# Kernel optimization log

Measured on AMD Instinct MI355X. Metric: run time of the kernel, lower is better.

The kernel has to match this reference:

```python
import jax, jax.numpy as jnp
import numpy as np

DEPTH = 6
DIM = 512
HEADS = 8
HD = DIM // HEADS          # head_dim = 64
HALF = HD // 4             # RoPE2D half_dim = 16
N = 85                     # 1 CLS + 4 + 16 + 64
TOKENS = [1, 4, 16, 64]
MAX_FREQ = 10.0
NEG = -1e30


def _build_mask():
    bounds = np.cumsum([0] + TOKENS)
    M = np.array([[1, 0, 0, 1], [1, 1, 0, 0], [1, 0, 1, 0], [0, 0, 0, 1]])
    m = np.full((N, N), NEG, np.float32)
    for i in range(4):
        for j in range(4):
            if M[i, j]:
                m[bounds[i]:bounds[i + 1], bounds[j]:bounds[j + 1]] = 0.0
    return jnp.asarray(m)

MASK = _build_mask()
FREQS = jnp.exp(jnp.arange(HALF, dtype=jnp.float32) * (-np.log(MAX_FREQ) / HALF))


def _centers():
    allc = []
    for g in (2, 4, 8):
        step = 1.0 / g
        off = step / 2
        ys, xs = np.meshgrid(np.arange(g), np.arange(g), indexing='ij')
        c = np.stack([off + xs * step, off + ys * step], axis=-1).reshape(-1, 2)
        allc.append(c)
    return jnp.asarray(np.concatenate(allc, 0), dtype=jnp.float32)


def _ln(x, w, b):
    mu = x.mean(-1, keepdims=True)
    var = x.var(-1, keepdims=True)
    return (x - mu) / jnp.sqrt(var + 1e-5) * w + b


def _rope(t, coords):
    # t: [B, H, M, HD] patch tokens (CLS excluded); coords: [M, 2]
    two_pi = 2.0 * jnp.pi
    ang_x = coords[:, 0:1] * FREQS[None, :] * two_pi   # [M, HALF]
    ang_y = coords[:, 1:2] * FREQS[None, :] * two_pi
    cx, sx = jnp.cos(ang_x), jnp.sin(ang_x)
    cy, sy = jnp.cos(ang_y), jnp.sin(ang_y)
    t = t.reshape(t.shape[:-1] + (4, HALF))
    x0, x1, x2, x3 = t[..., 0, :], t[..., 1, :], t[..., 2, :], t[..., 3, :]
    r = jnp.stack([x0 * cx - x1 * sx, x0 * sx + x1 * cx,
                   x2 * cy - x3 * sy, x2 * sy + x3 * cy], axis=-2)
    return r.reshape(r.shape[:-2] + (HD,))


def _attn(x, coords, qkv_w, qkv_b, proj_w, proj_b):
    B = x.shape[0]
    qkv = (x @ qkv_w + qkv_b).reshape(B, N, 3, HEADS, HD).transpose(2, 0, 3, 1, 4)
    q, k, v = qkv[0], qkv[1], qkv[2]   # each [B, H, N, HD]
    q = jnp.concatenate([q[:, :, :1], _rope(q[:, :, 1:], coords)], axis=2)
    k = jnp.concatenate([k[:, :, :1], _rope(k[:, :, 1:], coords)], axis=2)
    scores = jnp.einsum('bhqd,bhkd->bhqk', q, k) * (HD ** -0.5) + MASK
    a = jax.nn.softmax(scores, axis=-1)
    out = jnp.einsum('bhqk,bhkd->bhqd', a, v).transpose(0, 2, 1, 3).reshape(B, N, DIM)
    return out @ proj_w + proj_b


def _forward(x, coords, ln1_w, ln1_b, qkv_w, qkv_b, proj_w, proj_b,
             ln2_w, ln2_b, fc1_w, fc1_b, fc2_w, fc2_b, lnf_w, lnf_b):
    for l in range(DEPTH):
        h = _ln(x, ln1_w[l], ln1_b[l])
        x = x + _attn(h, coords, qkv_w[l], qkv_b[l], proj_w[l], proj_b[l])
        h = _ln(x, ln2_w[l], ln2_b[l])
        h = jax.nn.gelu(h @ fc1_w[l] + fc1_b[l], approximate=False)  # torch nn.GELU = erf
        x = x + h @ fc2_w[l] + fc2_b[l]
    return _ln(x, lnf_w, lnf_b)


def setup_inputs() -> dict:
    key = jax.random.key(0)
    ks = jax.random.split(key, 5)
    B = 512
    def w(k, shape, s=0.02):
        return jax.random.normal(k, shape, jnp.float32) * s
    return {
        'x': jax.random.normal(ks[0], (B, N, DIM), jnp.float32),
        'coords': _centers(),
        'ln1_w': jnp.ones((DEPTH, DIM), jnp.float32),
        'ln1_b': jnp.zeros((DEPTH, DIM), jnp.float32),
        'qkv_w': w(ks[1], (DEPTH, DIM, 3 * DIM)),
        'qkv_b': jnp.zeros((DEPTH, 3 * DIM), jnp.float32),
        'proj_w': w(ks[2], (DEPTH, DIM, DIM)),
        'proj_b': jnp.zeros((DEPTH, DIM), jnp.float32),
        'ln2_w': jnp.ones((DEPTH, DIM), jnp.float32),
        'ln2_b': jnp.zeros((DEPTH, DIM), jnp.float32),
        'fc1_w': w(ks[3], (DEPTH, DIM, 4 * DIM)),
        'fc1_b': jnp.zeros((DEPTH, 4 * DIM), jnp.float32),
        'fc2_w': w(ks[4], (DEPTH, 4 * DIM, DIM)),
        'fc2_b': jnp.zeros((DEPTH, DIM), jnp.float32),
        'lnf_w': jnp.ones((DIM,), jnp.float32),
        'lnf_b': jnp.zeros((DIM,), jnp.float32),
    }


def reference(x, coords, ln1_w, ln1_b, qkv_w, qkv_b, proj_w, proj_b,
              ln2_w, ln2_b, fc1_w, fc1_b, fc2_w, fc2_b, lnf_w, lnf_b):
    return _forward(x, coords, ln1_w, ln1_b, qkv_w, qkv_b, proj_w, proj_b,
                    ln2_w, ln2_b, fc1_w, fc1_b, fc2_w, fc2_b, lnf_w, lnf_b)
```

## Files before the change

### kernel.cpp

```cpp
#include <hip/hip_runtime.h>
#include <hip/hip_bf16.h>

typedef unsigned short u16;
typedef unsigned int u32;
typedef __attribute__((ext_vector_type(8))) short short8;
typedef __attribute__((ext_vector_type(4))) float floatx4;

#define MTOT 43520
#define DIMM 512
#define NHEAD 8

__device__ __forceinline__ float b2f(u16 u) { return __uint_as_float(((unsigned)u) << 16); }
__device__ __forceinline__ u16 f2b(float f) {
  unsigned u = __float_as_uint(f);
  return (u16)((u + 0x7FFFu + ((u >> 16) & 1u)) >> 16);
}

__device__ __forceinline__ void gld16(void* lds, const void* g) {
  __builtin_amdgcn_global_load_lds(
      (const __attribute__((address_space(1))) u32*)g,
      (__attribute__((address_space(3))) u32*)lds, 16, 0, 0);
}

__global__ __launch_bounds__(256) void transpose_conv(const float* __restrict__ in,
    u16* __restrict__ out, int K, int N)
{
  const float* W  = in  + (size_t)blockIdx.z * K * N;
  u16*         Wt = out + (size_t)blockIdx.z * K * N;
  int n0 = blockIdx.x * 64, k0 = blockIdx.y * 64;
  int t = threadIdx.x;
  #pragma unroll
  for (int i = 0; i < 2; i++) {
    int task = t + i * 256;
    int n = task >> 3, kc = (task & 7) * 8;
    u16 tmp[8];
    #pragma unroll
    for (int j = 0; j < 8; j++)
      tmp[j] = f2b(W[(size_t)(k0 + kc + j) * N + n0 + n]);
    *(uint4*)&Wt[(size_t)(n0 + n) * K + k0 + kc] = *(uint4*)tmp;
  }
}

template<int OUTF32>
__global__ __launch_bounds__(256) void ln_kernel(const float* __restrict__ x,
    const float* __restrict__ w, const float* __restrict__ b, void* __restrict__ out)
{
  int row  = blockIdx.x * 4 + (threadIdx.x >> 6);
  int lane = threadIdx.x & 63;
  const float* xr = x + (size_t)row * DIMM;
  float4 a = ((const float4*)xr)[lane * 2];
  float4 c = ((const float4*)xr)[lane * 2 + 1];
  float f[8] = { a.x, a.y, a.z, a.w, c.x, c.y, c.z, c.w };

  float s = 0.f, ss = 0.f;
  #pragma unroll
  for (int i = 0; i < 8; i++) { s += f[i]; ss += f[i] * f[i]; }
  #pragma unroll
  for (int off = 32; off > 0; off >>= 1) {
    s  += __shfl_xor(s,  off);
    ss += __shfl_xor(ss, off);
  }
  float mu  = s * (1.f / 512.f);
  float var = ss * (1.f / 512.f) - mu * mu;
  float rs  = rsqrtf(var + 1e-5f);

  float4 w0 = ((const float4*)w)[lane * 2], w1 = ((const float4*)w)[lane * 2 + 1];
  float4 b0 = ((const float4*)b)[lane * 2], b1 = ((const float4*)b)[lane * 2 + 1];
  float wv[8] = { w0.x, w0.y, w0.z, w0.w, w1.x, w1.y, w1.z, w1.w };
  float bv[8] = { b0.x, b0.y, b0.z, b0.w, b1.x, b1.y, b1.z, b1.w };

  if (OUTF32) {
    float res[8];
    #pragma unroll
    for (int i = 0; i < 8; i++) res[i] = (f[i] - mu) * rs * wv[i] + bv[i];
    float* orow = (float*)out + (size_t)row * DIMM;
    ((float4*)orow)[lane * 2]     = *(float4*)&res[0];
    ((float4*)orow)[lane * 2 + 1] = *(float4*)&res[4];
  } else {
    u16 res[8];
    #pragma unroll
    for (int i = 0; i < 8; i++) res[i] = f2b((f[i] - mu) * rs * wv[i] + bv[i]);
    ((uint4*)((u16*)out + (size_t)row * DIMM))[lane] = *(uint4*)res;
  }
}

template<int EPI>
__global__ __launch_bounds__(512, 2) void gemm256(
    const u16* __restrict__ A, const u16* __restrict__ Bt,
    const float* __restrict__ bias, const float* __restrict__ resid,
    void* __restrict__ Cv, int Nd, int K, int gx)
{
  __shared__ u16 As[2][2][128][64];
  __shared__ u16 Bs[2][2][128][64];

  int nwg  = gridDim.x;
  int orig = blockIdx.x;
  int xcd = orig & 7, cidx = orig >> 3;
  int qq = nwg >> 3, rr8 = nwg & 7;
  int nid = (xcd < rr8 ? xcd * (qq + 1) : rr8 * (qq + 1) + (xcd - rr8) * qq) + cidx;
  int bx = nid % gx, by = nid / gx;
  int m0 = by * 256, n0 = bx * 256;

  int t = threadIdx.x;
  int w = t >> 6, l = t & 63;
  int wr = w >> 2, wc = w & 3, quad = l >> 4, l16 = l & 15;
  int KT = K >> 6;

  int Rb = 8 * w + (l >> 3);
  int slog8 = (((l & 7) ^ ((l >> 3) & 7)) << 3);
  const u16* gAm = A  + (size_t)m0 * K + slog8;
  const u16* gBn = Bt + (size_t)n0 * K + slog8;
  int sx = l16 & 7;

  auto STAGE = [&](int ktj, int h) {
    int c = ktj & 1;
    u16* lb = (h < 2) ? &As[c][h & 1][0][0] : &Bs[c][h & 1][0][0];
    const u16* g = ((h < 2) ? gAm : gBn) + (size_t)((h & 1) * 128 + Rb) * K + ktj * 64;
    gld16(lb + w * 512,       g);
    gld16(lb + (8 + w) * 512, g + (size_t)64 * K);
  };

  STAGE(0, 0); STAGE(0, 1); STAGE(0, 2); STAGE(0, 3);
  STAGE(1, 0); STAGE(1, 1);
  asm volatile("s_waitcnt vmcnt(4)" ::: "memory");
  __builtin_amdgcn_s_barrier();
  __builtin_amdgcn_sched_barrier(0);

  floatx4 zero = {0.f, 0.f, 0.f, 0.f};
  floatx4 acc[8][4];
  #pragma unroll
  for (int mt = 0; mt < 8; mt++)
    #pragma unroll
    for (int nt = 0; nt < 4; nt++) acc[mt][nt] = zero;

  for (int kt = 0; kt < KT; ++kt) {
    int c = kt & 1;
    const u16 (*Ah)[64] = As[c][wr];
    const u16 (*Bh)[64] = Bs[c][wc >> 1];
    int bl = (wc & 1) * 64;

    short8 af[8][2], bf[4][2];

    #pragma unroll
    for (int mt = 0; mt < 4; mt++)
      #pragma unroll
      for (int kk = 0; kk < 2; kk++)
        af[mt][kk] = *(const short8*)&Ah[mt * 16 + l16][((kk * 4 + quad) ^ sx) << 3];
    #pragma unroll
    for (int nt = 0; nt < 2; nt++)
      #pragma unroll
      for (int kk = 0; kk < 2; kk++)
        bf[nt][kk] = *(const short8*)&Bh[bl + nt * 16 + l16][((kk * 4 + quad) ^ sx) << 3];
    { int j = 4 * kt + 6; if (j < 4 * KT) STAGE(j >> 2, j & 3); }
    __builtin_amdgcn_s_barrier();
    __builtin_amdgcn_s_setprio(1);
    #pragma unroll
    for (int nt = 0; nt < 2; nt++)
      #pragma unroll
      for (int mt = 0; mt < 4; mt++)
        #pragma unroll
        for (int kk = 0; kk < 2; kk++)
          acc[mt][nt] = __builtin_amdgcn_mfma_f32_16x16x32_bf16(af[mt][kk], bf[nt][kk], acc[mt][nt], 0, 0, 0);
    __builtin_amdgcn_s_setprio(0);
    __builtin_amdgcn_s_barrier();

    #pragma unroll
    for (int mt = 4; mt < 8; mt++)
      #pragma unroll
      for (int kk = 0; kk < 2; kk++)
        af[mt][kk] = *(const short8*)&Ah[mt * 16 + l16][((kk * 4 + quad) ^ sx) << 3];
    #pragma unroll
    for (int nt = 2; nt < 4; nt++)
      #pragma unroll
      for (int kk = 0; kk < 2; kk++)
        bf[nt][kk] = *(const short8*)&Bh[bl + nt * 16 + l16][((kk * 4 + quad) ^ sx) << 3];
    { int j = 4 * kt + 7; if (j < 4 * KT) STAGE(j >> 2, j & 3); }
    __builtin_amdgcn_s_barrier();
    __builtin_amdgcn_s_setprio(1);
    #pragma unroll
    for (int nt = 2; nt < 4; nt++)
      #pragma unroll
      for (int mt = 4; mt < 8; mt++)
        #pragma unroll
        for (int kk = 0; kk < 2; kk++)
          acc[mt][nt] = __builtin_amdgcn_mfma_f32_16x16x32_bf16(af[mt][kk], bf[nt][kk], acc[mt][nt], 0, 0, 0);
    __builtin_amdgcn_s_setprio(0);
    __builtin_amdgcn_s_barrier();

    { int j = 4 * kt + 8; if (j < 4 * KT) STAGE(j >> 2, j & 3); }
    __builtin_amdgcn_s_barrier();
    __builtin_amdgcn_s_setprio(1);
    #pragma unroll
    for (int nt = 2; nt < 4; nt++)
      #pragma unroll
      for (int mt = 0; mt < 4; mt++)
        #pragma unroll
        for (int kk = 0; kk < 2; kk++)
          acc[mt][nt] = __builtin_amdgcn_mfma_f32_16x16x32_bf16(af[mt][kk], bf[nt][kk], acc[mt][nt], 0, 0, 0);
    __builtin_amdgcn_s_setprio(0);
    __builtin_amdgcn_s_barrier();

    { int j = 4 * kt + 9; if (j < 4 * KT) STAGE(j >> 2, j & 3); }
    __builtin_amdgcn_s_barrier();
    __builtin_amdgcn_s_setprio(1);
    #pragma unroll
    for (int nt = 0; nt < 2; nt++)
      #pragma unroll
      for (int mt = 4; mt < 8; mt++)
        #pragma unroll
        for (int kk = 0; kk < 2; kk++)
          acc[mt][nt] = __builtin_amdgcn_mfma_f32_16x16x32_bf16(af[mt][kk], bf[nt][kk], acc[mt][nt], 0, 0, 0);
    __builtin_amdgcn_s_setprio(0);

    if (kt < KT - 1) {
      if (kt == KT - 2) asm volatile("s_waitcnt vmcnt(0)" ::: "memory");
      else              asm volatile("s_waitcnt vmcnt(4)" ::: "memory");
      __builtin_amdgcn_s_barrier();
      __builtin_amdgcn_sched_barrier(0);
    }
  }

  #pragma unroll
  for (int mt = 0; mt < 8; mt++) {
    #pragma unroll
    for (int nt = 0; nt < 4; nt++) {
      int nc = n0 + wc * 64 + nt * 16 + l16;
      float bv = bias[nc];
      #pragma unroll
      for (int r = 0; r < 4; r++) {
        int mr = m0 + wr * 128 + mt * 16 + quad * 4 + r;
        size_t idx = (size_t)mr * Nd + nc;
        float v = acc[mt][nt][r] + bv;
        if constexpr (EPI == 1) {
          ((float*)Cv)[idx] = v + resid[idx];
        } else if constexpr (EPI == 2) {
          v = 0.5f * v * (1.f + erff(v * 0.70710678118654752f));
          ((u16*)Cv)[idx] = f2b(v);
        } else {
          ((u16*)Cv)[idx] = f2b(v);
        }
      }
    }
  }
}

__device__ __forceinline__ int grp(int tk) { return tk == 0 ? 0 : (tk < 5 ? 1 : (tk < 21 ? 2 : 3)); }

__global__ __launch_bounds__(256) void attn_kernel(const u16* __restrict__ qkv,
    const float* __restrict__ coords, u16* __restrict__ out)
{
  __shared__ u16 Qs[96 * 72];
  __shared__ u16 Ks[96 * 72];
  __shared__ u16 Vt[64 * 104];
  __shared__ u16 Pb[96 * 104];

  int b = blockIdx.x >> 3, h = blockIdx.x & 7;
  int tid = threadIdx.x;
  const u16* base = qkv + ((size_t)b * 85) * 1536 + h * 64;

  for (int idx = tid; idx < 96 * 64; idx += 256) {
    int tk = idx >> 6, d = idx & 63;
    float qv = 0.f, kv = 0.f; u16 vv = 0;
    if (tk < 85) {
      const u16* qp = base + (size_t)tk * 1536;
      vv = qp[1024 + d];
      if (tk == 0) {
        qv = b2f(qp[d]); kv = b2f(qp[512 + d]);
      } else {
        int j = d & 15, q4 = d >> 4;
        float coord = coords[(tk - 1) * 2 + (q4 >> 1)];
        float freq = __expf((float)j * -0.14391156831212787f);
        float ang = coord * freq * 6.283185307179586f;
        float sn, cs; __sincosf(ang, &sn, &cs);
        int p0 = ((q4 & 2) << 4) + j, p1 = p0 + 16;
        float a0 = b2f(qp[p0]),       a1 = b2f(qp[p1]);
        float k0 = b2f(qp[512 + p0]), k1 = b2f(qp[512 + p1]);
        if (q4 & 1) { qv = a0 * sn + a1 * cs; kv = k0 * sn + k1 * cs; }
        else        { qv = a0 * cs - a1 * sn; kv = k0 * cs - k1 * sn; }
      }
    }
    Qs[tk * 72 + d] = f2b(qv);
    Ks[tk * 72 + d] = f2b(kv);
    Vt[d * 104 + tk] = vv;
  }
  __syncthreads();

  int wave = tid >> 6, lane = tid & 63, quad = lane >> 4, l16 = lane & 15;
  const unsigned MBITS = 0x8539u;
  floatx4 zero = {0.f, 0.f, 0.f, 0.f};

  int nb = (wave < 2) ? 2 : 1;
  for (int bi = 0; bi < nb; bi++) {
    int band = (bi == 0) ? wave : wave + 4;

    short8 a0 = *(const short8*)&Qs[(band * 16 + l16) * 72 + quad * 8];
    short8 a1 = *(const short8*)&Qs[(band * 16 + l16) * 72 + 32 + quad * 8];
    floatx4 s[6];
    #pragma unroll
    for (int nt = 0; nt < 6; nt++) {
      short8 b0 = *(const short8*)&Ks[(nt * 16 + l16) * 72 + quad * 8];
      short8 b1 = *(const short8*)&Ks[(nt * 16 + l16) * 72 + 32 + quad * 8];
      floatx4 tmp = __builtin_amdgcn_mfma_f32_16x16x32_bf16(a0, b0, zero, 0, 0, 0);
      s[nt] = __builtin_amdgcn_mfma_f32_16x16x32_bf16(a1, b1, tmp, 0, 0, 0);
    }

    int rb = band * 16 + quad * 4;
    #pragma unroll
    for (int r = 0; r < 4; r++) {
      int row = rb + r, gr = grp(row);
      float mx = -3.4e38f;
      #pragma unroll
      for (int nt = 0; nt < 6; nt++) {
        int col = nt * 16 + l16;
        float m = (col < 85 && ((MBITS >> (gr * 4 + grp(col))) & 1)) ? 0.f : -1e30f;
        s[nt][r] = s[nt][r] * 0.125f + m;
        mx = fmaxf(mx, s[nt][r]);
      }
      #pragma unroll
      for (int off = 1; off < 16; off <<= 1) mx = fmaxf(mx, __shfl_xor(mx, off));
      float sum = 0.f;
      #pragma unroll
      for (int nt = 0; nt < 6; nt++) { s[nt][r] = __expf(s[nt][r] - mx); sum += s[nt][r]; }
      #pragma unroll
      for (int off = 1; off < 16; off <<= 1) sum += __shfl_xor(sum, off);
      float inv = 1.f / sum;
      #pragma unroll
      for (int nt = 0; nt < 6; nt++)
        Pb[row * 104 + nt * 16 + l16] = f2b(s[nt][r] * inv);
    }

    floatx4 o[4];
    #pragma unroll
    for (int nt2 = 0; nt2 < 4; nt2++) o[nt2] = zero;
    #pragma unroll
    for (int ks = 0; ks < 3; ks++) {
      short8 pa = *(const short8*)&Pb[(band * 16 + l16) * 104 + ks * 32 + quad * 8];
      #pragma unroll
      for (int nt2 = 0; nt2 < 4; nt2++) {
        short8 vb = *(const short8*)&Vt[(nt2 * 16 + l16) * 104 + ks * 32 + quad * 8];
        o[nt2] = __builtin_amdgcn_mfma_f32_16x16x32_bf16(pa, vb, o[nt2], 0, 0, 0);
      }
    }
    #pragma unroll
    for (int nt2 = 0; nt2 < 4; nt2++) {
      #pragma unroll
      for (int r = 0; r < 4; r++) {
        int row = rb + r;
        if (row < 85)
          out[((size_t)b * 85 + row) * 512 + h * 64 + nt2 * 16 + l16] = f2b(o[nt2][r]);
      }
    }
  }
}

extern "C" void kernel_launch(void* const* d_in, const int* in_sizes, int n_in,
                              void* d_out, int out_size, void* d_ws, size_t ws_size,
                              hipStream_t stream) {
  (void)in_sizes; (void)n_in; (void)out_size; (void)ws_size;
  const float* x_in   = (const float*)d_in[0];
  const float* coords = (const float*)d_in[1];
  const float* ln1_w  = (const float*)d_in[2];
  const float* ln1_b  = (const float*)d_in[3];
  const float* qkv_w  = (const float*)d_in[4];
  const float* qkv_b  = (const float*)d_in[5];
  const float* proj_w = (const float*)d_in[6];
  const float* proj_b = (const float*)d_in[7];
  const float* ln2_w  = (const float*)d_in[8];
  const float* ln2_b  = (const float*)d_in[9];
  const float* fc1_w  = (const float*)d_in[10];
  const float* fc1_b  = (const float*)d_in[11];
  const float* fc2_w  = (const float*)d_in[12];
  const float* fc2_b  = (const float*)d_in[13];
  const float* lnf_w  = (const float*)d_in[14];
  const float* lnf_b  = (const float*)d_in[15];

  float* xb = (float*)d_ws;
  u16*   hb = (u16*)(xb + (size_t)MTOT * 512);
  u16*   qb = hb + (size_t)MTOT * 512;
  u16*   wbuf = qb + (size_t)MTOT * 2048;
  u16* wq = wbuf;
  u16* wp = wq + (size_t)6 * 512 * 1536;
  u16* w1 = wp + (size_t)6 * 512 * 512;
  u16* w2 = w1 + (size_t)6 * 512 * 2048;

  dim3 blk(256);
  dim3 blkg(512);
  transpose_conv<<<dim3(1536 / 64, 512 / 64, 6), blk, 0, stream>>>(qkv_w, wq, 512, 1536);
  transpose_conv<<<dim3(512 / 64, 512 / 64, 6), blk, 0, stream>>>(proj_w, wp, 512, 512);
  transpose_conv<<<dim3(2048 / 64, 512 / 64, 6), blk, 0, stream>>>(fc1_w, w1, 512, 2048);
  transpose_conv<<<dim3(512 / 64, 2048 / 64, 6), blk, 0, stream>>>(fc2_w, w2, 2048, 512);

  const int MT = MTOT / 256;
  for (int l = 0; l < 6; l++) {
    const float* xcur = (l == 0) ? x_in : xb;
    ln_kernel<0><<<MTOT / 4, blk, 0, stream>>>(xcur, ln1_w + l * 512, ln1_b + l * 512, hb);
    gemm256<0><<<6 * MT, blkg, 0, stream>>>(
        hb, wq + (size_t)l * 512 * 1536, qkv_b + (size_t)l * 1536, nullptr, qb, 1536, 512, 6);
    attn_kernel<<<512 * NHEAD, blk, 0, stream>>>(qb, coords, hb);
    gemm256<1><<<2 * MT, blkg, 0, stream>>>(
        hb, wp + (size_t)l * 512 * 512, proj_b + (size_t)l * 512, xcur, xb, 512, 512, 2);
    ln_kernel<0><<<MTOT / 4, blk, 0, stream>>>(xb, ln2_w + l * 512, ln2_b + l * 512, hb);
    gemm256<2><<<8 * MT, blkg, 0, stream>>>(
        hb, w1 + (size_t)l * 512 * 2048, fc1_b + (size_t)l * 2048, nullptr, qb, 2048, 512, 8);
    gemm256<1><<<2 * MT, blkg, 0, stream>>>(
        qb, w2 + (size_t)l * 2048 * 512, fc2_b + (size_t)l * 512, xb, xb, 512, 2048, 2);
  }
  ln_kernel<1><<<MTOT / 4, blk, 0, stream>>>(xb, lnf_w, lnf_b, d_out);
}
```

Measured before the change: 4.240 ms.

## Make GEMM persistent with a fixed grid and prefetch the next tile

Turns gemm256 into a persistent kernel. A fixed grid of 256 workgroups loops over output tiles with a stride of the grid size. While the current tile's last k-steps and epilogue run, the first LDS stages of the next tile are issued, so the next tile's prologue loads overlap the current tile's compute and stores. In exchange, only one 512-thread workgroup per CU is resident where there used to be up to two, and proj/fc2 now need two uneven rounds of tiles, which can leave CUs idle or reduce latency hiding.

```diff
diff --git a/kernel.cpp b/kernel.cpp
--- a/kernel.cpp
+++ b/kernel.cpp
@@ -88,7 +88,7 @@
 __global__ __launch_bounds__(512, 2) void gemm256(
     const u16* __restrict__ A, const u16* __restrict__ Bt,
     const float* __restrict__ bias, const float* __restrict__ resid,
-    void* __restrict__ Cv, int Nd, int K, int gx)
+    void* __restrict__ Cv, int Nd, int K, int gx, int ntiles)
 {
   __shared__ u16 As[2][2][128][64];
   __shared__ u16 Bs[2][2][128][64];
@@ -98,8 +98,7 @@
   int xcd = orig & 7, cidx = orig >> 3;
   int qq = nwg >> 3, rr8 = nwg & 7;
   int nid = (xcd < rr8 ? xcd * (qq + 1) : rr8 * (qq + 1) + (xcd - rr8) * qq) + cidx;
-  int bx = nid % gx, by = nid / gx;
-  int m0 = by * 256, n0 = bx * 256;
+  if (nid >= ntiles) return;
 
   int t = threadIdx.x;
   int w = t >> 6, l = t & 63;
@@ -108,139 +107,177 @@
 
   int Rb = 8 * w + (l >> 3);
   int slog8 = (((l & 7) ^ ((l >> 3) & 7)) << 3);
-  const u16* gAm = A  + (size_t)m0 * K + slog8;
-  const u16* gBn = Bt + (size_t)n0 * K + slog8;
   int sx = l16 & 7;
 
-  auto STAGE = [&](int ktj, int h) {
+  int tcur = nid;
+  int by = tcur / gx, bx = tcur - by * gx;
+  int m0 = by * 256, n0 = bx * 256;
+  const u16* gAc = A  + (size_t)m0 * K + slog8;
+  const u16* gBc = Bt + (size_t)n0 * K + slog8;
+  int tn = tcur + nwg;
+  bool havenext = tn < ntiles;
+  int m0n = m0, n0n = n0;
+  const u16* gAn = gAc;
+  const u16* gBn = gBc;
+  if (havenext) {
+    int byn = tn / gx, bxn = tn - byn * gx;
+    m0n = byn * 256; n0n = bxn * 256;
+    gAn = A  + (size_t)m0n * K + slog8;
+    gBn = Bt + (size_t)n0n * K + slog8;
+  }
+
+  auto STAGE = [&](int j) {
+    int ktj = j >> 2, h = j & 3;
+    bool nxt = ktj >= KT;
+    if (nxt && !havenext) return;
+    int kk = nxt ? ktj - KT : ktj;
+    const u16* gbase = (h < 2) ? (nxt ? gAn : gAc) : (nxt ? gBn : gBc);
     int c = ktj & 1;
     u16* lb = (h < 2) ? &As[c][h & 1][0][0] : &Bs[c][h & 1][0][0];
-    const u16* g = ((h < 2) ? gAm : gBn) + (size_t)((h & 1) * 128 + Rb) * K + ktj * 64;
+    const u16* g = gbase + (size_t)((h & 1) * 128 + Rb) * K + kk * 64;
     gld16(lb + w * 512,       g);
     gld16(lb + (8 + w) * 512, g + (size_t)64 * K);
   };
 
-  STAGE(0, 0); STAGE(0, 1); STAGE(0, 2); STAGE(0, 3);
-  STAGE(1, 0); STAGE(1, 1);
+  STAGE(0); STAGE(1); STAGE(2); STAGE(3); STAGE(4); STAGE(5);
   asm volatile("s_waitcnt vmcnt(4)" ::: "memory");
   __builtin_amdgcn_s_barrier();
   __builtin_amdgcn_sched_barrier(0);
 
   floatx4 zero = {0.f, 0.f, 0.f, 0.f};
   floatx4 acc[8][4];
-  #pragma unroll
-  for (int mt = 0; mt < 8; mt++)
-    #pragma unroll
-    for (int nt = 0; nt < 4; nt++) acc[mt][nt] = zero;
-
-  for (int kt = 0; kt < KT; ++kt) {
-    int c = kt & 1;
-    const u16 (*Ah)[64] = As[c][wr];
-    const u16 (*Bh)[64] = Bs[c][wc >> 1];
-    int bl = (wc & 1) * 64;
-
-    short8 af[8][2], bf[4][2];
-
-    #pragma unroll
-    for (int mt = 0; mt < 4; mt++)
-      #pragma unroll
-      for (int kk = 0; kk < 2; kk++)
-        af[mt][kk] = *(const short8*)&Ah[mt * 16 + l16][((kk * 4 + quad) ^ sx) << 3];
-    #pragma unroll
-    for (int nt = 0; nt < 2; nt++)
-      #pragma unroll
-      for (int kk = 0; kk < 2; kk++)
-        bf[nt][kk] = *(const short8*)&Bh[bl + nt * 16 + l16][((kk * 4 + quad) ^ sx) << 3];
-    { int j = 4 * kt + 6; if (j < 4 * KT) STAGE(j >> 2, j & 3); }
+
+  while (true) {
+    #pragma unroll
+    for (int mt = 0; mt < 8; mt++)
+      #pragma unroll
+      for (int nt = 0; nt < 4; nt++) acc[mt][nt] = zero;
+
+    for (int kt = 0; kt < KT; ++kt) {
+      int c = kt & 1;
+      const u16 (*Ah)[64] = As[c][wr];
+      const u16 (*Bh)[64] = Bs[c][wc >> 1];
+      int bl = (wc & 1) * 64;
+
+      short8 af[8][2], bf[4][2];
+
+      #pragma unroll
+      for (int mt = 0; mt < 4; mt++)
+        #pragma unroll
+        for (int kk = 0; kk < 2; kk++)
+          af[mt][kk] = *(const short8*)&Ah[mt * 16 + l16][((kk * 4 + quad) ^ sx) << 3];
+      #pragma unroll
+      for (int nt = 0; nt < 2; nt++)
+        #pragma unroll
+        for (int kk = 0; kk < 2; kk++)
+          bf[nt][kk] = *(const short8*)&Bh[bl + nt * 16 + l16][((kk * 4 + quad) ^ sx) << 3];
+      STAGE(4 * kt + 6);
+      __builtin_amdgcn_s_barrier();
+      __builtin_amdgcn_s_setprio(1);
+      #pragma unroll
+      for (int nt = 0; nt < 2; nt++)
+        #pragma unroll
+        for (int mt = 0; mt < 4; mt++)
+          #pragma unroll
+          for (int kk = 0; kk < 2; kk++)
+            acc[mt][nt] = __builtin_amdgcn_mfma_f32_16x16x32_bf16(af[mt][kk], bf[nt][kk], acc[mt][nt], 0, 0, 0);
+      __builtin_amdgcn_s_setprio(0);
+      __builtin_amdgcn_s_barrier();
+
+      #pragma unroll
+      for (int mt = 4; mt < 8; mt++)
+        #pragma unroll
+        for (int kk = 0; kk < 2; kk++)
+          af[mt][kk] = *(const short8*)&Ah[mt * 16 + l16][((kk * 4 + quad) ^ sx) << 3];
+      #pragma unroll
+      for (int nt = 2; nt < 4; nt++)
+        #pragma unroll
+        for (int kk = 0; kk < 2; kk++)
+          bf[nt][kk] = *(const short8*)&Bh[bl + nt * 16 + l16][((kk * 4 + quad) ^ sx) << 3];
+      STAGE(4 * kt + 7);
+      __builtin_amdgcn_s_barrier();
+      __builtin_amdgcn_s_setprio(1);
+      #pragma unroll
+      for (int nt = 2; nt < 4; nt++)
+        #pragma unroll
+        for (int mt = 4; mt < 8; mt++)
+          #pragma unroll
+          for (int kk = 0; kk < 2; kk++)
+            acc[mt][nt] = __builtin_amdgcn_mfma_f32_16x16x32_bf16(af[mt][kk], bf[nt][kk], acc[mt][nt], 0, 0, 0);
+      __builtin_amdgcn_s_setprio(0);
+      __builtin_amdgcn_s_barrier();
+
+      STAGE(4 * kt + 8);
+      __builtin_amdgcn_s_barrier();
+      __builtin_amdgcn_s_setprio(1);
+      #pragma unroll
+      for (int nt = 2; nt < 4; nt++)
+        #pragma unroll
+        for (int mt = 0; mt < 4; mt++)
+          #pragma unroll
+          for (int kk = 0; kk < 2; kk++)
+            acc[mt][nt] = __builtin_amdgcn_mfma_f32_16x16x32_bf16(af[mt][kk], bf[nt][kk], acc[mt][nt], 0, 0, 0);
+      __builtin_amdgcn_s_setprio(0);
+      __builtin_amdgcn_s_barrier();
+
+      STAGE(4 * kt + 9);
+      __builtin_amdgcn_s_barrier();
+      __builtin_amdgcn_s_setprio(1);
+      #pragma unroll
+      for (int nt = 0; nt < 2; nt++)
+        #pragma unroll
+        for (int mt = 4; mt < 8; mt++)
+          #pragma unroll
+          for (int kk = 0; kk < 2; kk++)
+            acc[mt][nt] = __builtin_amdgcn_mfma_f32_16x16x32_bf16(af[mt][kk], bf[nt][kk], acc[mt][nt], 0, 0, 0);
+      __builtin_amdgcn_s_setprio(0);
+
+      if (kt < KT - 1) {
+        if (kt == KT - 2 && !havenext) asm volatile("s_waitcnt vmcnt(0)" ::: "memory");
+        else                           asm volatile("s_waitcnt vmcnt(4)" ::: "memory");
+        __builtin_amdgcn_s_barrier();
+        __builtin_amdgcn_sched_barrier(0);
+      }
+    }
+
+    if (havenext) asm volatile("s_waitcnt vmcnt(4)" ::: "memory");
+
+    #pragma unroll
+    for (int mt = 0; mt < 8; mt++) {
+      #pragma unroll
+      for (int nt = 0; nt < 4; nt++) {
+        int nc = n0 + wc * 64 + nt * 16 + l16;
+        float bv = bias[nc];
+        #pragma unroll
+        for (int r = 0; r < 4; r++) {
+          int mr = m0 + wr * 128 + mt * 16 + quad * 4 + r;
+          size_t idx = (size_t)mr * Nd + nc;
+          float v = acc[mt][nt][r] + bv;
+          if constexpr (EPI == 1) {
+            ((float*)Cv)[idx] = v + resid[idx];
+          } else if constexpr (EPI == 2) {
+            v = 0.5f * v * (1.f + erff(v * 0.70710678118654752f));
+            ((u16*)Cv)[idx] = f2b(v);
+          } else {
+            ((u16*)Cv)[idx] = f2b(v);
+          }
+        }
+      }
+    }
+
+    if (!havenext) break;
+
+    m0 = m0n; n0 = n0n; gAc = gAn; gBc = gBn;
+    tn += nwg;
+    havenext = tn < ntiles;
+    if (havenext) {
+      int byn = tn / gx, bxn = tn - byn * gx;
+      m0n = byn * 256; n0n = bxn * 256;
+      gAn = A  + (size_t)m0n * K + slog8;
+      gBn = Bt + (size_t)n0n * K + slog8;
+    }
     __builtin_amdgcn_s_barrier();
-    __builtin_amdgcn_s_setprio(1);
-    #pragma unroll
-    for (int nt = 0; nt < 2; nt++)
-      #pragma unroll
-      for (int mt = 0; mt < 4; mt++)
-        #pragma unroll
-        for (int kk = 0; kk < 2; kk++)
-          acc[mt][nt] = __builtin_amdgcn_mfma_f32_16x16x32_bf16(af[mt][kk], bf[nt][kk], acc[mt][nt], 0, 0, 0);
-    __builtin_amdgcn_s_setprio(0);
-    __builtin_amdgcn_s_barrier();
-
-    #pragma unroll
-    for (int mt = 4; mt < 8; mt++)
-      #pragma unroll
-      for (int kk = 0; kk < 2; kk++)
-        af[mt][kk] = *(const short8*)&Ah[mt * 16 + l16][((kk * 4 + quad) ^ sx) << 3];
-    #pragma unroll
-    for (int nt = 2; nt < 4; nt++)
-      #pragma unroll
-      for (int kk = 0; kk < 2; kk++)
-        bf[nt][kk] = *(const short8*)&Bh[bl + nt * 16 + l16][((kk * 4 + quad) ^ sx) << 3];
-    { int j = 4 * kt + 7; if (j < 4 * KT) STAGE(j >> 2, j & 3); }
-    __builtin_amdgcn_s_barrier();
-    __builtin_amdgcn_s_setprio(1);
-    #pragma unroll
-    for (int nt = 2; nt < 4; nt++)
-      #pragma unroll
-      for (int mt = 4; mt < 8; mt++)
-        #pragma unroll
-        for (int kk = 0; kk < 2; kk++)
-          acc[mt][nt] = __builtin_amdgcn_mfma_f32_16x16x32_bf16(af[mt][kk], bf[nt][kk], acc[mt][nt], 0, 0, 0);
-    __builtin_amdgcn_s_setprio(0);
-    __builtin_amdgcn_s_barrier();
-
-    { int j = 4 * kt + 8; if (j < 4 * KT) STAGE(j >> 2, j & 3); }
-    __builtin_amdgcn_s_barrier();
-    __builtin_amdgcn_s_setprio(1);
-    #pragma unroll
-    for (int nt = 2; nt < 4; nt++)
-      #pragma unroll
-      for (int mt = 0; mt < 4; mt++)
-        #pragma unroll
-        for (int kk = 0; kk < 2; kk++)
-          acc[mt][nt] = __builtin_amdgcn_mfma_f32_16x16x32_bf16(af[mt][kk], bf[nt][kk], acc[mt][nt], 0, 0, 0);
-    __builtin_amdgcn_s_setprio(0);
-    __builtin_amdgcn_s_barrier();
-
-    { int j = 4 * kt + 9; if (j < 4 * KT) STAGE(j >> 2, j & 3); }
-    __builtin_amdgcn_s_barrier();
-    __builtin_amdgcn_s_setprio(1);
-    #pragma unroll
-    for (int nt = 0; nt < 2; nt++)
-      #pragma unroll
-      for (int mt = 4; mt < 8; mt++)
-        #pragma unroll
-        for (int kk = 0; kk < 2; kk++)
-          acc[mt][nt] = __builtin_amdgcn_mfma_f32_16x16x32_bf16(af[mt][kk], bf[nt][kk], acc[mt][nt], 0, 0, 0);
-    __builtin_amdgcn_s_setprio(0);
-
-    if (kt < KT - 1) {
-      if (kt == KT - 2) asm volatile("s_waitcnt vmcnt(0)" ::: "memory");
-      else              asm volatile("s_waitcnt vmcnt(4)" ::: "memory");
-      __builtin_amdgcn_s_barrier();
-      __builtin_amdgcn_sched_barrier(0);
-    }
-  }
-
-  #pragma unroll
-  for (int mt = 0; mt < 8; mt++) {
-    #pragma unroll
-    for (int nt = 0; nt < 4; nt++) {
-      int nc = n0 + wc * 64 + nt * 16 + l16;
-      float bv = bias[nc];
-      #pragma unroll
-      for (int r = 0; r < 4; r++) {
-        int mr = m0 + wr * 128 + mt * 16 + quad * 4 + r;
-        size_t idx = (size_t)mr * Nd + nc;
-        float v = acc[mt][nt][r] + bv;
-        if constexpr (EPI == 1) {
-          ((float*)Cv)[idx] = v + resid[idx];
-        } else if constexpr (EPI == 2) {
-          v = 0.5f * v * (1.f + erff(v * 0.70710678118654752f));
-          ((u16*)Cv)[idx] = f2b(v);
-        } else {
-          ((u16*)Cv)[idx] = f2b(v);
-        }
-      }
-    }
+    __builtin_amdgcn_sched_barrier(0);
   }
 }
 
@@ -391,19 +428,20 @@
   transpose_conv<<<dim3(512 / 64, 2048 / 64, 6), blk, 0, stream>>>(fc2_w, w2, 2048, 512);
 
   const int MT = MTOT / 256;
+  const int PG = 256;
   for (int l = 0; l < 6; l++) {
     const float* xcur = (l == 0) ? x_in : xb;
     ln_kernel<0><<<MTOT / 4, blk, 0, stream>>>(xcur, ln1_w + l * 512, ln1_b + l * 512, hb);
-    gemm256<0><<<6 * MT, blkg, 0, stream>>>(
-        hb, wq + (size_t)l * 512 * 1536, qkv_b + (size_t)l * 1536, nullptr, qb, 1536, 512, 6);
+    gemm256<0><<<PG, blkg, 0, stream>>>(
+        hb, wq + (size_t)l * 512 * 1536, qkv_b + (size_t)l * 1536, nullptr, qb, 1536, 512, 6, 6 * MT);
     attn_kernel<<<512 * NHEAD, blk, 0, stream>>>(qb, coords, hb);
-    gemm256<1><<<2 * MT, blkg, 0, stream>>>(
-        hb, wp + (size_t)l * 512 * 512, proj_b + (size_t)l * 512, xcur, xb, 512, 512, 2);
+    gemm256<1><<<PG, blkg, 0, stream>>>(
+        hb, wp + (size_t)l * 512 * 512, proj_b + (size_t)l * 512, xcur, xb, 512, 512, 2, 2 * MT);
     ln_kernel<0><<<MTOT / 4, blk, 0, stream>>>(xb, ln2_w + l * 512, ln2_b + l * 512, hb);
-    gemm256<2><<<8 * MT, blkg, 0, stream>>>(
-        hb, w1 + (size_t)l * 512 * 2048, fc1_b + (size_t)l * 2048, nullptr, qb, 2048, 512, 8);
-    gemm256<1><<<2 * MT, blkg, 0, stream>>>(
-        qb, w2 + (size_t)l * 2048 * 512, fc2_b + (size_t)l * 512, xb, xb, 512, 2048, 2);
+    gemm256<2><<<PG, blkg, 0, stream>>>(
+        hb, w1 + (size_t)l * 512 * 2048, fc1_b + (size_t)l * 2048, nullptr, qb, 2048, 512, 8, 8 * MT);
+    gemm256<1><<<PG, blkg, 0, stream>>>(
+        qb, w2 + (size_t)l * 2048 * 512, fc2_b + (size_t)l * 512, xb, xb, 512, 2048, 2, 2 * MT);
   }
   ln_kernel<1><<<MTOT / 4, blk, 0, stream>>>(xb, lnf_w, lnf_b, d_out);
 }
```

Result: faster. 4.028 ms (-5.0%).

## Replace 256x256 GEMM tile kernel with 128x128 tile, 256-thread variant

Applied to the files above, without the earlier changes.

The 512-thread 256x256-tile GEMM becomes a 256-thread 128x128-tile kernel with a 2x2 wave layout and 4x4 MFMA accumulators per wave. The staging pipeline shrinks from four sub-phases per k-step to two, prefetching B for k+1 and A for k+2 into double-buffered LDS. Grid sizes for all four GEMM launches are rescaled to match. This aims at better occupancy and smaller tail effects, but gives up data reuse per loaded tile and adds more blocks and global traffic.

```diff
diff --git a/kernel.cpp b/kernel.cpp
--- a/kernel.cpp
+++ b/kernel.cpp
@@ -85,39 +85,42 @@
 }
 
 template<int EPI>
-__global__ __launch_bounds__(512, 2) void gemm256(
+__global__ __launch_bounds__(256, 2) void gemm128(
     const u16* __restrict__ A, const u16* __restrict__ Bt,
     const float* __restrict__ bias, const float* __restrict__ resid,
     void* __restrict__ Cv, int Nd, int K, int gx)
 {
-  __shared__ u16 As[2][2][128][64];
-  __shared__ u16 Bs[2][2][128][64];
+  __shared__ u16 As[2][128][64];
+  __shared__ u16 Bs[2][128][64];
 
   int nwg  = gridDim.x;
   int orig = blockIdx.x;
   int xcd = orig & 7, cidx = orig >> 3;
   int qq = nwg >> 3, rr8 = nwg & 7;
   int nid = (xcd < rr8 ? xcd * (qq + 1) : rr8 * (qq + 1) + (xcd - rr8) * qq) + cidx;
-  int bx = nid % gx, by = nid / gx;
-  int m0 = by * 256, n0 = bx * 256;
+  int by = nid / gx, bx = nid - by * gx;
+  int m0 = by * 128, n0 = bx * 128;
 
   int t = threadIdx.x;
   int w = t >> 6, l = t & 63;
-  int wr = w >> 2, wc = w & 3, quad = l >> 4, l16 = l & 15;
+  int wr = w >> 1, wc = w & 1, quad = l >> 4, l16 = l & 15;
   int KT = K >> 6;
 
-  int Rb = 8 * w + (l >> 3);
+  int Rb = 16 * w + (l >> 3);
   int slog8 = (((l & 7) ^ ((l >> 3) & 7)) << 3);
-  const u16* gAm = A  + (size_t)m0 * K + slog8;
-  const u16* gBn = Bt + (size_t)n0 * K + slog8;
   int sx = l16 & 7;
+  const u16* gA = A  + (size_t)m0 * K + slog8;
+  const u16* gB = Bt + (size_t)n0 * K + slog8;
 
   auto STAGE = [&](int ktj, int h) {
+    if (ktj >= KT) return;
     int c = ktj & 1;
-    u16* lb = (h < 2) ? &As[c][h & 1][0][0] : &Bs[c][h & 1][0][0];
-    const u16* g = ((h < 2) ? gAm : gBn) + (size_t)((h & 1) * 128 + Rb) * K + ktj * 64;
-    gld16(lb + w * 512,       g);
-    gld16(lb + (8 + w) * 512, g + (size_t)64 * K);
+    u16* lb = (h < 2) ? &As[c][0][0] : &Bs[c][0][0];
+    const u16* gbase = (h < 2) ? gA : gB;
+    int half = (h & 1) << 6;
+    const u16* g = gbase + (size_t)(half + Rb) * K + ktj * 64;
+    gld16(lb + (half + 16 * w) * 64,     g);
+    gld16(lb + (half + 16 * w + 8) * 64, g + (size_t)8 * K);
   };
 
   STAGE(0, 0); STAGE(0, 1); STAGE(0, 2); STAGE(0, 3);
@@ -127,31 +130,31 @@
   __builtin_amdgcn_sched_barrier(0);
 
   floatx4 zero = {0.f, 0.f, 0.f, 0.f};
-  floatx4 acc[8][4];
-  #pragma unroll
-  for (int mt = 0; mt < 8; mt++)
+  floatx4 acc[4][4];
+  #pragma unroll
+  for (int mt = 0; mt < 4; mt++)
     #pragma unroll
     for (int nt = 0; nt < 4; nt++) acc[mt][nt] = zero;
 
   for (int kt = 0; kt < KT; ++kt) {
     int c = kt & 1;
-    const u16 (*Ah)[64] = As[c][wr];
-    const u16 (*Bh)[64] = Bs[c][wc >> 1];
-    int bl = (wc & 1) * 64;
-
-    short8 af[8][2], bf[4][2];
+    const u16 (*Ah)[64] = As[c];
+    const u16 (*Bh)[64] = Bs[c];
+
+    short8 af[4][2], bf[4][2];
 
     #pragma unroll
     for (int mt = 0; mt < 4; mt++)
       #pragma unroll
       for (int kk = 0; kk < 2; kk++)
-        af[mt][kk] = *(const short8*)&Ah[mt * 16 + l16][((kk * 4 + quad) ^ sx) << 3];
+        af[mt][kk] = *(const short8*)&Ah[wr * 64 + mt * 16 + l16][((kk * 4 + quad) ^ sx) << 3];
     #pragma unroll
     for (int nt = 0; nt < 2; nt++)
       #pragma unroll
       for (int kk = 0; kk < 2; kk++)
-        bf[nt][kk] = *(const short8*)&Bh[bl + nt * 16 + l16][((kk * 4 + quad) ^ sx) << 3];
-    { int j = 4 * kt + 6; if (j < 4 * KT) STAGE(j >> 2, j & 3); }
+        bf[nt][kk] = *(const short8*)&Bh[wc * 64 + nt * 16 + l16][((kk * 4 + quad) ^ sx) << 3];
+    STAGE(kt + 1, 2);
+    STAGE(kt + 1, 3);
     __builtin_amdgcn_s_barrier();
     __builtin_amdgcn_s_setprio(1);
     #pragma unroll
@@ -165,30 +168,12 @@
     __builtin_amdgcn_s_barrier();
 
     #pragma unroll
-    for (int mt = 4; mt < 8; mt++)
+    for (int nt = 2; nt < 4; nt++)
       #pragma unroll
       for (int kk = 0; kk < 2; kk++)
-        af[mt][kk] = *(const short8*)&Ah[mt * 16 + l16][((kk * 4 + quad) ^ sx) << 3];
-    #pragma unroll
-    for (int nt = 2; nt < 4; nt++)
-      #pragma unroll
-      for (int kk = 0; kk < 2; kk++)
-        bf[nt][kk] = *(const short8*)&Bh[bl + nt * 16 + l16][((kk * 4 + quad) ^ sx) << 3];
-    { int j = 4 * kt + 7; if (j < 4 * KT) STAGE(j >> 2, j & 3); }
-    __builtin_amdgcn_s_barrier();
-    __builtin_amdgcn_s_setprio(1);
-    #pragma unroll
-    for (int nt = 2; nt < 4; nt++)
-      #pragma unroll
-      for (int mt = 4; mt < 8; mt++)
-        #pragma unroll
-        for (int kk = 0; kk < 2; kk++)
-          acc[mt][nt] = __builtin_amdgcn_mfma_f32_16x16x32_bf16(af[mt][kk], bf[nt][kk], acc[mt][nt], 0, 0, 0);
-    __builtin_amdgcn_s_setprio(0);
-    __builtin_amdgcn_s_barrier();
-
-    { int j = 4 * kt + 8; if (j < 4 * KT) STAGE(j >> 2, j & 3); }
-    __builtin_amdgcn_s_barrier();
+        bf[nt][kk] = *(const short8*)&Bh[wc * 64 + nt * 16 + l16][((kk * 4 + quad) ^ sx) << 3];
+    STAGE(kt + 2, 0);
+    STAGE(kt + 2, 1);
     __builtin_amdgcn_s_setprio(1);
     #pragma unroll
     for (int nt = 2; nt < 4; nt++)
@@ -198,19 +183,6 @@
         for (int kk = 0; kk < 2; kk++)
           acc[mt][nt] = __builtin_amdgcn_mfma_f32_16x16x32_bf16(af[mt][kk], bf[nt][kk], acc[mt][nt], 0, 0, 0);
     __builtin_amdgcn_s_setprio(0);
-    __builtin_amdgcn_s_barrier();
-
-    { int j = 4 * kt + 9; if (j < 4 * KT) STAGE(j >> 2, j & 3); }
-    __builtin_amdgcn_s_barrier();
-    __builtin_amdgcn_s_setprio(1);
-    #pragma unroll
-    for (int nt = 0; nt < 2; nt++)
-      #pragma unroll
-      for (int mt = 4; mt < 8; mt++)
-        #pragma unroll
-        for (int kk = 0; kk < 2; kk++)
-          acc[mt][nt] = __builtin_amdgcn_mfma_f32_16x16x32_bf16(af[mt][kk], bf[nt][kk], acc[mt][nt], 0, 0, 0);
-    __builtin_amdgcn_s_setprio(0);
 
     if (kt < KT - 1) {
       if (kt == KT - 2) asm volatile("s_waitcnt vmcnt(0)" ::: "memory");
@@ -221,14 +193,14 @@
   }
 
   #pragma unroll
-  for (int mt = 0; mt < 8; mt++) {
+  for (int mt = 0; mt < 4; mt++) {
     #pragma unroll
     for (int nt = 0; nt < 4; nt++) {
       int nc = n0 + wc * 64 + nt * 16 + l16;
       float bv = bias[nc];
       #pragma unroll
       for (int r = 0; r < 4; r++) {
-        int mr = m0 + wr * 128 + mt * 16 + quad * 4 + r;
+        int mr = m0 + wr * 64 + mt * 16 + quad * 4 + r;
         size_t idx = (size_t)mr * Nd + nc;
         float v = acc[mt][nt][r] + bv;
         if constexpr (EPI == 1) {
@@ -384,26 +356,25 @@
   u16* w2 = w1 + (size_t)6 * 512 * 2048;
 
   dim3 blk(256);
-  dim3 blkg(512);
   transpose_conv<<<dim3(1536 / 64, 512 / 64, 6), blk, 0, stream>>>(qkv_w, wq, 512, 1536);
   transpose_conv<<<dim3(512 / 64, 512 / 64, 6), blk, 0, stream>>>(proj_w, wp, 512, 512);
   transpose_conv<<<dim3(2048 / 64, 512 / 64, 6), blk, 0, stream>>>(fc1_w, w1, 512, 2048);
   transpose_conv<<<dim3(512 / 64, 2048 / 64, 6), blk, 0, stream>>>(fc2_w, w2, 2048, 512);
 
-  const int MT = MTOT / 256;
+  const int MT = MTOT / 128;
   for (int l = 0; l < 6; l++) {
     const float* xcur = (l == 0) ? x_in : xb;
     ln_kernel<0><<<MTOT / 4, blk, 0, stream>>>(xcur, ln1_w + l * 512, ln1_b + l * 512, hb);
-    gemm256<0><<<6 * MT, blkg, 0, stream>>>(
-        hb, wq + (size_t)l * 512 * 1536, qkv_b + (size_t)l * 1536, nullptr, qb, 1536, 512, 6);
+    gemm128<0><<<12 * MT, blk, 0, stream>>>(
+        hb, wq + (size_t)l * 512 * 1536, qkv_b + (size_t)l * 1536, nullptr, qb, 1536, 512, 12);
     attn_kernel<<<512 * NHEAD, blk, 0, stream>>>(qb, coords, hb);
-    gemm256<1><<<2 * MT, blkg, 0, stream>>>(
-        hb, wp + (size_t)l * 512 * 512, proj_b + (size_t)l * 512, xcur, xb, 512, 512, 2);
+    gemm128<1><<<4 * MT, blk, 0, stream>>>(
+        hb, wp + (size_t)l * 512 * 512, proj_b + (size_t)l * 512, xcur, xb, 512, 512, 4);
     ln_kernel<0><<<MTOT / 4, blk, 0, stream>>>(xb, ln2_w + l * 512, ln2_b + l * 512, hb);
-    gemm256<2><<<8 * MT, blkg, 0, stream>>>(
-        hb, w1 + (size_t)l * 512 * 2048, fc1_b + (size_t)l * 2048, nullptr, qb, 2048, 512, 8);
-    gemm256<1><<<2 * MT, blkg, 0, stream>>>(
-        qb, w2 + (size_t)l * 2048 * 512, fc2_b + (size_t)l * 512, xb, xb, 512, 2048, 2);
+    gemm128<2><<<16 * MT, blk, 0, stream>>>(
+        hb, w1 + (size_t)l * 512 * 2048, fc1_b + (size_t)l * 2048, nullptr, qb, 2048, 512, 16);
+    gemm128<1><<<4 * MT, blk, 0, stream>>>(
+        qb, w2 + (size_t)l * 2048 * 512, fc2_b + (size_t)l * 512, xb, xb, 512, 2048, 4);
   }
   ln_kernel<1><<<MTOT / 4, blk, 0, stream>>>(xb, lnf_w, lnf_b, d_out);
 }
```

Result: faster. 3.818 ms (-9.9%).
